# Performance work log

Measured on AMD Instinct MI355X. Metric: run time of the kernel, lower is better.

## Reference

```python
import jax, jax.numpy as jnp
import numpy as np

FEAT_DIM, PART_DIM, N_PARTS, N_EXPERTS, N_ALT = 384, 256, 8, 4, 4
CLUSTER_TEMP = 0.07
EXPERT_WARMUP = 8


def _ln(x, g, b, eps=1e-5):
    mu = x.mean(-1, keepdims=True)
    var = ((x - mu) ** 2).mean(-1, keepdims=True)
    return (x - mu) * jax.lax.rsqrt(var + eps) * g + b


def _l2norm(x, eps=1e-12):
    n = jnp.sqrt((x * x).sum(-1, keepdims=True))
    return x / jnp.maximum(n, eps)


def _gelu(x):
    return jax.nn.gelu(x, approximate=False)


def setup_inputs() -> dict:
    key = jax.random.key(0)
    ks = jax.random.split(key, 32)
    B, N = 256, 576
    s = lambda k, shp, sc=0.02: jax.random.normal(k, shp, jnp.float32) * sc
    inp = {
        'patch_features': jax.random.normal(ks[0], (B, N, FEAT_DIM), jnp.float32),
        'alt_idx': jax.random.randint(ks[1], (B,), 0, N_ALT, jnp.int32),
        'epoch': 0,
        # feat_proj: Linear(384,256) + LayerNorm(256) + GELU
        'w_proj': s(ks[2], (FEAT_DIM, PART_DIM)), 'b_proj': jnp.zeros((PART_DIM,)),
        'ln1_g': jnp.ones((PART_DIM,)), 'ln1_b': jnp.zeros((PART_DIM,)),
        # expert prototypes [E, K, D]
        'protos': s(ks[3], (N_EXPERTS, N_PARTS, PART_DIM)),
        # router
        'r_alt_emb': s(ks[4], (N_ALT, 64), 1.0),
        'r_wf': s(ks[5], (PART_DIM, 64)), 'r_bf': jnp.zeros((64,)),
        'r_w1': s(ks[6], (128, 64)), 'r_b1': jnp.zeros((64,)),
        'r_w2': s(ks[7], (64, N_EXPERTS)), 'r_b2': jnp.zeros((N_EXPERTS,)),
        # refine: LN + Linear(256,512) + GELU + Linear(512,256)
        'ref_ln_g': jnp.ones((PART_DIM,)), 'ref_ln_b': jnp.zeros((PART_DIM,)),
        'ref_w1': s(ks[8], (PART_DIM, 2 * PART_DIM)), 'ref_b1': jnp.zeros((2 * PART_DIM,)),
        'ref_w2': s(ks[9], (2 * PART_DIM, PART_DIM)), 'ref_b2': jnp.zeros((PART_DIM,)),
        # salience head: Linear(256,64)+GELU+Linear(64,1)+Sigmoid
        'sal_w1': s(ks[10], (PART_DIM, 64)), 'sal_b1': jnp.zeros((64,)),
        'sal_w2': s(ks[11], (64, 1)), 'sal_b2': jnp.zeros((1,)),
    }
    return inp


def reference(patch_features, alt_idx, epoch, w_proj, b_proj, ln1_g, ln1_b, protos,
              r_alt_emb, r_wf, r_bf, r_w1, r_b1, r_w2, r_b2,
              ref_ln_g, ref_ln_b, ref_w1, ref_b1, ref_w2, ref_b2,
              sal_w1, sal_b1, sal_w2, sal_b2):
    # --- feat projection ---
    feat = _gelu(_ln(patch_features @ w_proj + b_proj, ln1_g, ln1_b))  # [B,N,D]
    feat_stats = feat.mean(axis=1)  # [B,D]

    # --- router (AltitudeExpertRouter) ---
    warm = min(epoch / max(EXPERT_WARMUP, 1), 1.0)
    router_temp = 2.0 * (1.0 - warm) + 0.5 * warm
    f = jax.nn.relu(feat_stats @ r_wf + r_bf)            # [B,64]
    a = r_alt_emb[alt_idx]                               # [B,64]
    h = jax.nn.relu(jnp.concatenate([f, a], -1) @ r_w1 + r_b1)
    logits = (h @ r_w2 + r_b2) / router_temp             # [B,E]
    gate_weights = jax.nn.softmax(logits, axis=-1)

    # --- blended prototypes + soft assignment ---
    prototypes = jnp.einsum('be,ekd->bkd', gate_weights, protos)  # [B,K,D]
    sim = jnp.einsum('bnd,bkd->bnk', _l2norm(feat), _l2norm(prototypes)) / CLUSTER_TEMP
    assign = jax.nn.softmax(sim, axis=-1)                # [B,N,K]

    assign_t = jnp.swapaxes(assign, 1, 2)                # [B,K,N]
    mass = jnp.maximum(assign_t.sum(-1, keepdims=True), 1e-6)
    part_feat = jnp.einsum('bkn,bnd->bkd', assign_t, feat) / mass

    # --- refine residual ---
    r = _ln(part_feat, ref_ln_g, ref_ln_b)
    r = _gelu(r @ ref_w1 + ref_b1) @ ref_w2 + ref_b2
    part_feat = part_feat + r

    # --- salience ---
    salience = jax.nn.sigmoid(_gelu(part_feat @ sal_w1 + sal_b1) @ sal_w2 + sal_b2)[..., 0]

    return part_feat, assign, salience, feat, gate_weights


if __name__ == '__main__':
    out = reference(**setup_inputs())
    for o in out:
        print(o.shape, o.dtype)
```

## Files before the change

### kernel.cpp

```cpp
#include <hip/hip_runtime.h>
#include <hip/hip_bf16.h>
#include <math.h>

#define B_ 256
#define N_ 576
#define F_ 384
#define D_ 256
#define K_ 8

#define OFF_PART   0
#define OFF_ASSIGN 524288
#define OFF_SAL    1703936
#define OFF_FEAT   1705984
#define OFF_GATE   39454720

#define WS_STATS   0
#define WS_MACC    65536
#define WS_MASS    589824
#define WS_PROTON  591872
#define WS_BTW     1116160

using s16x8 = __attribute__((ext_vector_type(8))) short;
using f32x4 = __attribute__((ext_vector_type(4))) float;

__device__ __forceinline__ float gelu_exact(float x) {
    return 0.5f * x * (1.0f + erff(x * 0.70710678118654752f));
}

__device__ __forceinline__ unsigned short f2b(float f) {
    __hip_bfloat16 h = __float2bfloat16(f);
    unsigned short u;
    __builtin_memcpy(&u, &h, 2);
    return u;
}

__global__ void k0_zero(float* __restrict__ p, int n) {
    int i = blockIdx.x * blockDim.x + threadIdx.x;
    if (i < n) p[i] = 0.f;
}

__global__ void kB_conv(const float* __restrict__ w, unsigned short* __restrict__ bt) {
    int k = threadIdx.x;
    int n = blockIdx.x;
    bt[n * 384 + k] = f2b(w[k * 256 + n]);
}

__global__ __launch_bounds__(256, 3) void k1_pipe(
    const float* __restrict__ patch, const unsigned short* __restrict__ btw,
    const float* __restrict__ bias, const float* __restrict__ g,
    const float* __restrict__ bb, float* __restrict__ feat,
    float* __restrict__ stats)
{
    __shared__ __align__(16) unsigned short As[64 * 72];
    __shared__ __align__(16) unsigned short Bs[256 * 72];
    __shared__ float rsum[4][64];
    __shared__ float rsq[4][64];
    __shared__ float muS[64], rsS[64];

    const int t = threadIdx.x;
    const int w = t >> 6;
    const int lane = t & 63;
    const int l15 = lane & 15;
    const int l4 = lane >> 4;
    const size_t rowbase = (size_t)blockIdx.x * 64;
    const int bidx = blockIdx.x / 9;

    f32x4 acc[4][4];
#pragma unroll
    for (int m = 0; m < 4; ++m)
#pragma unroll
        for (int n = 0; n < 4; ++n)
            acc[m][n] = (f32x4){0.f, 0.f, 0.f, 0.f};

    const int ar = t >> 2;
    const int ak = (t & 3) * 16;
    const int brr = t >> 3;
    const int bk = (t & 7) * 8;

    const float* aptr = patch + (rowbase + ar) * F_ + ak;
    const unsigned short* bptr = btw + (size_t)brr * F_ + bk;

    float4 pa[4];
    s16x8 pb[8];

#pragma unroll
    for (int i = 0; i < 4; ++i) pa[i] = *(const float4*)(aptr + 4 * i);
#pragma unroll
    for (int p = 0; p < 8; ++p) pb[p] = *(const s16x8*)(bptr + (size_t)(32 * p) * F_);

    for (int c = 0; c < 6; ++c) {
        __syncthreads();
        {
            s16x8 c0, c1;
            c0[0] = (short)f2b(pa[0].x); c0[1] = (short)f2b(pa[0].y);
            c0[2] = (short)f2b(pa[0].z); c0[3] = (short)f2b(pa[0].w);
            c0[4] = (short)f2b(pa[1].x); c0[5] = (short)f2b(pa[1].y);
            c0[6] = (short)f2b(pa[1].z); c0[7] = (short)f2b(pa[1].w);
            c1[0] = (short)f2b(pa[2].x); c1[1] = (short)f2b(pa[2].y);
            c1[2] = (short)f2b(pa[2].z); c1[3] = (short)f2b(pa[2].w);
            c1[4] = (short)f2b(pa[3].x); c1[5] = (short)f2b(pa[3].y);
            c1[6] = (short)f2b(pa[3].z); c1[7] = (short)f2b(pa[3].w);
            *(s16x8*)&As[ar * 72 + ak] = c0;
            *(s16x8*)&As[ar * 72 + ak + 8] = c1;
#pragma unroll
            for (int p = 0; p < 8; ++p)
                *(s16x8*)&Bs[(brr + 32 * p) * 72 + bk] = pb[p];
        }
        __syncthreads();
        if (c < 5) {
            const int k1 = (c + 1) * 64;
#pragma unroll
            for (int i = 0; i < 4; ++i) pa[i] = *(const float4*)(aptr + k1 + 4 * i);
#pragma unroll
            for (int p = 0; p < 8; ++p) pb[p] = *(const s16x8*)(bptr + (size_t)(32 * p) * F_ + k1);
        }
#pragma unroll
        for (int kk = 0; kk < 2; ++kk) {
            const int kb = kk * 32 + l4 * 8;
            s16x8 afr[4], bfr[4];
#pragma unroll
            for (int m = 0; m < 4; ++m)
                afr[m] = *(const s16x8*)&As[(m * 16 + l15) * 72 + kb];
#pragma unroll
            for (int n = 0; n < 4; ++n)
                bfr[n] = *(const s16x8*)&Bs[(w * 64 + n * 16 + l15) * 72 + kb];
#pragma unroll
            for (int m = 0; m < 4; ++m)
#pragma unroll
                for (int n = 0; n < 4; ++n)
                    acc[m][n] = __builtin_amdgcn_mfma_f32_16x16x32_bf16(afr[m], bfr[n], acc[m][n], 0, 0, 0);
        }
    }

    float bv[4], gv[4], bbv[4];
#pragma unroll
    for (int n = 0; n < 4; ++n) {
        int col = w * 64 + n * 16 + l15;
        bv[n] = bias[col]; gv[n] = g[col]; bbv[n] = bb[col];
    }
#pragma unroll
    for (int m = 0; m < 4; ++m)
#pragma unroll
        for (int n = 0; n < 4; ++n)
#pragma unroll
            for (int r = 0; r < 4; ++r)
                acc[m][n][r] += bv[n];

    float ps[4][4], p2[4][4];
#pragma unroll
    for (int m = 0; m < 4; ++m)
#pragma unroll
        for (int r = 0; r < 4; ++r) {
            float s = 0.f, s2 = 0.f;
#pragma unroll
            for (int n = 0; n < 4; ++n) {
                float x = acc[m][n][r];
                s += x; s2 += x * x;
            }
            ps[m][r] = s; p2[m][r] = s2;
        }
#pragma unroll
    for (int m = 0; m < 4; ++m)
#pragma unroll
        for (int r = 0; r < 4; ++r) {
#pragma unroll
            for (int msk = 1; msk < 16; msk <<= 1) {
                ps[m][r] += __shfl_xor(ps[m][r], msk);
                p2[m][r] += __shfl_xor(p2[m][r], msk);
            }
        }
    if (l15 == 0) {
#pragma unroll
        for (int m = 0; m < 4; ++m)
#pragma unroll
            for (int r = 0; r < 4; ++r) {
                int row = m * 16 + l4 * 4 + r;
                rsum[w][row] = ps[m][r];
                rsq[w][row] = p2[m][r];
            }
    }
    __syncthreads();
    if (t < 64) {
        float s = rsum[0][t] + rsum[1][t] + rsum[2][t] + rsum[3][t];
        float q = rsq[0][t] + rsq[1][t] + rsq[2][t] + rsq[3][t];
        float mean = s * (1.f / 256.f);
        float var = q * (1.f / 256.f) - mean * mean;
        muS[t] = mean;
        rsS[t] = rsqrtf(var + 1e-5f);
    }
    __syncthreads();

    float cst[4] = {0.f, 0.f, 0.f, 0.f};
#pragma unroll
    for (int m = 0; m < 4; ++m)
#pragma unroll
        for (int r = 0; r < 4; ++r) {
            int row = m * 16 + l4 * 4 + r;
            float mu = muS[row], ri = rsS[row];
            float* fp = feat + (rowbase + row) * 256;
#pragma unroll
            for (int n = 0; n < 4; ++n) {
                int col = w * 64 + n * 16 + l15;
                float x = acc[m][n][r];
                float y = (x - mu) * ri * gv[n] + bbv[n];
                float z = gelu_exact(y);
                fp[col] = z;
                cst[n] += z;
            }
        }
#pragma unroll
    for (int n = 0; n < 4; ++n) {
        cst[n] += __shfl_xor(cst[n], 16);
        cst[n] += __shfl_xor(cst[n], 32);
    }
    if (l4 == 0) {
#pragma unroll
        for (int n = 0; n < 4; ++n)
            atomicAdd(&stats[bidx * 256 + w * 64 + n * 16 + l15], cst[n]);
    }
}

__global__ __launch_bounds__(256) void k3_router(
    const float* __restrict__ stats, const int* __restrict__ alt_idx,
    const int* __restrict__ epoch_p,
    const float* __restrict__ r_alt_emb, const float* __restrict__ r_wf,
    const float* __restrict__ r_bf, const float* __restrict__ r_w1,
    const float* __restrict__ r_b1, const float* __restrict__ r_w2,
    const float* __restrict__ r_b2, const float* __restrict__ protos,
    float* __restrict__ gate_out, float* __restrict__ proto_n)
{
    __shared__ float fs[256];
    __shared__ float cv[128];
    __shared__ float hb[64];
    __shared__ float lg[4];
    __shared__ float gate[4];
    __shared__ float pl[8 * 260];
    __shared__ float nrm[8];
    const int t = threadIdx.x, b = blockIdx.x;
    fs[t] = stats[b * D_ + t] * (1.f / (float)N_);
    __syncthreads();
    if (t < 64) {
        float a = 0.f;
        for (int d = 0; d < 256; ++d) a += fs[d] * r_wf[d * 64 + t];
        cv[t] = fmaxf(a + r_bf[t], 0.f);
    } else if (t < 128) {
        int alt = alt_idx[b];
        cv[t] = r_alt_emb[alt * 64 + (t - 64)];
    }
    __syncthreads();
    if (t < 64) {
        float a = 0.f;
        for (int d = 0; d < 128; ++d) a += cv[d] * r_w1[d * 64 + t];
        hb[t] = fmaxf(a + r_b1[t], 0.f);
    }
    __syncthreads();
    if (t < 4) {
        float a = 0.f;
        for (int d = 0; d < 64; ++d) a += hb[d] * r_w2[d * 4 + t];
        int ep = epoch_p[0];
        float warm = fminf((float)ep * (1.f / 8.f), 1.f);
        float temp = 2.f * (1.f - warm) + 0.5f * warm;
        lg[t] = (a + r_b2[t]) / temp;
    }
    __syncthreads();
    if (t == 0) {
        float m = fmaxf(fmaxf(lg[0], lg[1]), fmaxf(lg[2], lg[3]));
        float e0 = expf(lg[0] - m), e1 = expf(lg[1] - m);
        float e2 = expf(lg[2] - m), e3 = expf(lg[3] - m);
        float s = e0 + e1 + e2 + e3;
        gate[0] = e0 / s; gate[1] = e1 / s; gate[2] = e2 / s; gate[3] = e3 / s;
    }
    __syncthreads();
    if (t < 4) gate_out[b * 4 + t] = gate[t];
    float g0 = gate[0], g1 = gate[1], g2 = gate[2], g3 = gate[3];
#pragma unroll
    for (int k = 0; k < 8; ++k) {
        float p = g0 * protos[(0 * 8 + k) * 256 + t] + g1 * protos[(1 * 8 + k) * 256 + t]
                + g2 * protos[(2 * 8 + k) * 256 + t] + g3 * protos[(3 * 8 + k) * 256 + t];
        pl[k * 260 + t] = p;
    }
    __syncthreads();
    const int wave = t >> 6, lane = t & 63;
#pragma unroll
    for (int kk = 0; kk < 2; ++kk) {
        int k = wave * 2 + kk;
        float4 v = *(const float4*)(&pl[k * 260 + lane * 4]);
        float s2 = v.x * v.x + v.y * v.y + v.z * v.z + v.w * v.w;
#pragma unroll
        for (int m = 1; m < 64; m <<= 1) s2 += __shfl_xor(s2, m);
        if (lane == 0) nrm[k] = 1.f / fmaxf(sqrtf(s2), 1e-12f);
    }
    __syncthreads();
#pragma unroll
    for (int k = 0; k < 8; ++k)
        proto_n[((size_t)(b * 8 + k)) * 256 + t] = pl[k * 260 + t] * nrm[k];
}

__global__ __launch_bounds__(256) void k4_part(
    const float* __restrict__ feat, const float* __restrict__ proto_n,
    float* __restrict__ assign_out, float* __restrict__ macc_ws,
    float* __restrict__ mass_ws)
{
    __shared__ float pp[8 * 260];
    __shared__ float ft[16 * 260];
    __shared__ float asg[16 * 8];
    __shared__ float inrm[16];
    const int t = threadIdx.x, b = blockIdx.y;
    const int wave = t >> 6, lane = t & 63;
#pragma unroll
    for (int k = 0; k < 8; ++k) pp[k * 260 + t] = proto_n[((size_t)(b * 8 + k)) * 256 + t];
    float macc[8], mass[8];
#pragma unroll
    for (int k = 0; k < 8; ++k) { macc[k] = 0.f; mass[k] = 0.f; }
    const int sn = t >> 4;
    const int sk = (t >> 1) & 7;
    const int hf = t & 1;
    const int lc = (t & 15) * 4;
    const int t0 = blockIdx.x * 9;
    for (int tile = t0; tile < t0 + 9; ++tile) {
        int n0 = tile * 16;
        __syncthreads();
        const float* fsrc = feat + ((size_t)(b * N_ + n0 + sn) * D_) + lc;
#pragma unroll
        for (int i = 0; i < 4; ++i) {
            float4 v = *(const float4*)(fsrc + 64 * i);
            *(float4*)(&ft[sn * 260 + lc + 64 * i]) = v;
        }
        __syncthreads();
#pragma unroll
        for (int rr = 0; rr < 4; ++rr) {
            int n = wave * 4 + rr;
            float4 v = *(const float4*)(&ft[n * 260 + lane * 4]);
            float s2 = v.x * v.x + v.y * v.y + v.z * v.z + v.w * v.w;
#pragma unroll
            for (int m = 1; m < 64; m <<= 1) s2 += __shfl_xor(s2, m);
            if (lane == 0) inrm[n] = 1.f / fmaxf(sqrtf(s2), 1e-12f);
        }
        __syncthreads();
        {
            const float4* fp = (const float4*)(&ft[sn * 260 + hf * 128]);
            const float4* qp = (const float4*)(&pp[sk * 260 + hf * 128]);
            float a = 0.f;
#pragma unroll 8
            for (int dd = 0; dd < 32; ++dd) {
                float4 fv = fp[dd], qv = qp[dd];
                a += fv.x * qv.x + fv.y * qv.y + fv.z * qv.z + fv.w * qv.w;
            }
            a += __shfl_xor(a, 1);
            float sim = a * inrm[sn] * (1.f / 0.07f);
            float m = sim;
            m = fmaxf(m, __shfl_xor(m, 2));
            m = fmaxf(m, __shfl_xor(m, 4));
            m = fmaxf(m, __shfl_xor(m, 8));
            float p = expf(sim - m);
            float s = p;
            s += __shfl_xor(s, 2);
            s += __shfl_xor(s, 4);
            s += __shfl_xor(s, 8);
            float av = p / s;
            if (hf == 0) assign_out[((size_t)(b * N_ + n0 + sn)) * 8 + sk] = av;
            asg[sn * 8 + sk] = av;
        }
        __syncthreads();
#pragma unroll 4
        for (int nn = 0; nn < 16; ++nn) {
            float4 a03 = *(const float4*)(&asg[nn * 8]);
            float4 a47 = *(const float4*)(&asg[nn * 8 + 4]);
            float fv = ft[nn * 260 + t];
            macc[0] += a03.x * fv; macc[1] += a03.y * fv;
            macc[2] += a03.z * fv; macc[3] += a03.w * fv;
            macc[4] += a47.x * fv; macc[5] += a47.y * fv;
            macc[6] += a47.z * fv; macc[7] += a47.w * fv;
            mass[0] += a03.x; mass[1] += a03.y; mass[2] += a03.z; mass[3] += a03.w;
            mass[4] += a47.x; mass[5] += a47.y; mass[6] += a47.z; mass[7] += a47.w;
        }
    }
#pragma unroll
    for (int k = 0; k < 8; ++k)
        atomicAdd(&macc_ws[((size_t)(b * 8 + k)) * 256 + t], macc[k]);
    if (t == 0) {
        atomicAdd(&mass_ws[b * 8 + 0], mass[0]);
        atomicAdd(&mass_ws[b * 8 + 1], mass[1]);
        atomicAdd(&mass_ws[b * 8 + 2], mass[2]);
        atomicAdd(&mass_ws[b * 8 + 3], mass[3]);
        atomicAdd(&mass_ws[b * 8 + 4], mass[4]);
        atomicAdd(&mass_ws[b * 8 + 5], mass[5]);
        atomicAdd(&mass_ws[b * 8 + 6], mass[6]);
        atomicAdd(&mass_ws[b * 8 + 7], mass[7]);
    }
}

__global__ __launch_bounds__(256) void k5_refine(
    const float* __restrict__ macc_ws, const float* __restrict__ mass_ws,
    const float* __restrict__ ref_ln_g, const float* __restrict__ ref_ln_b,
    const float* __restrict__ ref_w1, const float* __restrict__ ref_b1,
    const float* __restrict__ ref_w2, const float* __restrict__ ref_b2,
    const float* __restrict__ sal_w1, const float* __restrict__ sal_b1,
    const float* __restrict__ sal_w2, const float* __restrict__ sal_b2,
    float* __restrict__ part_out, float* __restrict__ sal_out)
{
    __shared__ float raw[8 * 256];
    __shared__ float rn[8 * 256];
    __shared__ float h1[8 * 512];
    __shared__ float pf[8 * 256];
    __shared__ float s1[8 * 64];
    __shared__ float mu[8], rs[8];
    const int t = threadIdx.x, b = blockIdx.x;
    const int wave = t >> 6, lane = t & 63;
#pragma unroll
    for (int r = 0; r < 8; ++r) {
        float mm = fmaxf(mass_ws[b * 8 + r], 1e-6f);
        raw[r * 256 + t] = macc_ws[((size_t)(b * 8 + r)) * 256 + t] / mm;
    }
    __syncthreads();
#pragma unroll
    for (int rr = 0; rr < 2; ++rr) {
        int r = wave + rr * 4;
        float4 v = *(const float4*)(&raw[r * 256 + lane * 4]);
        float s = v.x + v.y + v.z + v.w;
        float s2 = v.x * v.x + v.y * v.y + v.z * v.z + v.w * v.w;
#pragma unroll
        for (int m = 1; m < 64; m <<= 1) { s += __shfl_xor(s, m); s2 += __shfl_xor(s2, m); }
        if (lane == 0) {
            float mean = s * (1.f / 256.f);
            float var = s2 * (1.f / 256.f) - mean * mean;
            mu[r] = mean;
            rs[r] = rsqrtf(var + 1e-5f);
        }
    }
    __syncthreads();
    {
        float gg = ref_ln_g[t], bbv = ref_ln_b[t];
#pragma unroll
        for (int r = 0; r < 8; ++r) {
            float x = raw[r * 256 + t];
            rn[r * 256 + t] = (x - mu[r]) * rs[r] * gg + bbv;
        }
    }
    __syncthreads();
    {
        float acca[8], accb[8];
#pragma unroll
        for (int r = 0; r < 8; ++r) { acca[r] = 0.f; accb[r] = 0.f; }
        for (int d = 0; d < 256; d += 4) {
            float4 rv[8];
#pragma unroll
            for (int r = 0; r < 8; ++r) rv[r] = *(const float4*)(&rn[r * 256 + d]);
            float wa0 = ref_w1[(size_t)(d + 0) * 512 + t], wb0 = ref_w1[(size_t)(d + 0) * 512 + t + 256];
            float wa1 = ref_w1[(size_t)(d + 1) * 512 + t], wb1 = ref_w1[(size_t)(d + 1) * 512 + t + 256];
            float wa2 = ref_w1[(size_t)(d + 2) * 512 + t], wb2 = ref_w1[(size_t)(d + 2) * 512 + t + 256];
            float wa3 = ref_w1[(size_t)(d + 3) * 512 + t], wb3 = ref_w1[(size_t)(d + 3) * 512 + t + 256];
#pragma unroll
            for (int r = 0; r < 8; ++r) {
                acca[r] += rv[r].x * wa0 + rv[r].y * wa1 + rv[r].z * wa2 + rv[r].w * wa3;
                accb[r] += rv[r].x * wb0 + rv[r].y * wb1 + rv[r].z * wb2 + rv[r].w * wb3;
            }
        }
        float b1a = ref_b1[t], b1b = ref_b1[t + 256];
#pragma unroll
        for (int r = 0; r < 8; ++r) {
            h1[r * 512 + t] = gelu_exact(acca[r] + b1a);
            h1[r * 512 + t + 256] = gelu_exact(accb[r] + b1b);
        }
    }
    __syncthreads();
    {
        float acc2[8];
#pragma unroll
        for (int r = 0; r < 8; ++r) acc2[r] = 0.f;
        for (int d = 0; d < 512; d += 4) {
            float4 hv[8];
#pragma unroll
            for (int r = 0; r < 8; ++r) hv[r] = *(const float4*)(&h1[r * 512 + d]);
            float w0 = ref_w2[(size_t)(d + 0) * 256 + t];
            float w1v = ref_w2[(size_t)(d + 1) * 256 + t];
            float w2v = ref_w2[(size_t)(d + 2) * 256 + t];
            float w3v = ref_w2[(size_t)(d + 3) * 256 + t];
#pragma unroll
            for (int r = 0; r < 8; ++r)
                acc2[r] += hv[r].x * w0 + hv[r].y * w1v + hv[r].z * w2v + hv[r].w * w3v;
        }
        float b2v = ref_b2[t];
#pragma unroll
        for (int r = 0; r < 8; ++r) {
            float v = raw[r * 256 + t] + acc2[r] + b2v;
            part_out[((size_t)(b * 8 + r)) * 256 + t] = v;
            pf[r * 256 + t] = v;
        }
    }
    __syncthreads();
    for (int o = t; o < 512; o += 256) {
        int r = o >> 6, j = o & 63;
        float a = 0.f;
        for (int d = 0; d < 256; d += 4) {
            float4 v = *(const float4*)(&pf[r * 256 + d]);
            a += v.x * sal_w1[(d + 0) * 64 + j] + v.y * sal_w1[(d + 1) * 64 + j]
               + v.z * sal_w1[(d + 2) * 64 + j] + v.w * sal_w1[(d + 3) * 64 + j];
        }
        s1[o] = gelu_exact(a + sal_b1[j]);
    }
    __syncthreads();
    if (t < 8) {
        float a = 0.f;
#pragma unroll 8
        for (int d = 0; d < 64; ++d) a += s1[t * 64 + d] * sal_w2[d];
        float x = a + sal_b2[0];
        sal_out[b * 8 + t] = 1.f / (1.f + expf(-x));
    }
}

extern "C" void kernel_launch(void* const* d_in, const int* in_sizes, int n_in,
                              void* d_out, int out_size, void* d_ws, size_t ws_size,
                              hipStream_t stream) {
    const float* patch    = (const float*)d_in[0];
    const int*   alt_idx  = (const int*)d_in[1];
    const int*   epoch    = (const int*)d_in[2];
    const float* w_proj   = (const float*)d_in[3];
    const float* b_proj   = (const float*)d_in[4];
    const float* ln1_g    = (const float*)d_in[5];
    const float* ln1_b    = (const float*)d_in[6];
    const float* protos   = (const float*)d_in[7];
    const float* r_alt    = (const float*)d_in[8];
    const float* r_wf     = (const float*)d_in[9];
    const float* r_bf     = (const float*)d_in[10];
    const float* r_w1     = (const float*)d_in[11];
    const float* r_b1     = (const float*)d_in[12];
    const float* r_w2     = (const float*)d_in[13];
    const float* r_b2     = (const float*)d_in[14];
    const float* ref_ln_g = (const float*)d_in[15];
    const float* ref_ln_b = (const float*)d_in[16];
    const float* ref_w1   = (const float*)d_in[17];
    const float* ref_b1   = (const float*)d_in[18];
    const float* ref_w2   = (const float*)d_in[19];
    const float* ref_b2   = (const float*)d_in[20];
    const float* sal_w1   = (const float*)d_in[21];
    const float* sal_b1   = (const float*)d_in[22];
    const float* sal_w2   = (const float*)d_in[23];
    const float* sal_b2   = (const float*)d_in[24];

    float* out = (float*)d_out;
    float* wsf = (float*)d_ws;
    float* stats   = wsf + WS_STATS;
    float* macc    = wsf + WS_MACC;
    float* mass    = wsf + WS_MASS;
    float* proto_n = wsf + WS_PROTON;
    unsigned short* btw = (unsigned short*)(wsf + WS_BTW);

    k0_zero<<<dim3((65536 + 524288 + 2048 + 255) / 256), dim3(256), 0, stream>>>(stats, 65536 + 524288 + 2048);
    kB_conv<<<dim3(256), dim3(384), 0, stream>>>(w_proj, btw);
    k1_pipe<<<dim3(2304), dim3(256), 0, stream>>>(patch, btw, b_proj, ln1_g, ln1_b,
                                                  out + OFF_FEAT, stats);
    k3_router<<<dim3(256), dim3(256), 0, stream>>>(stats, alt_idx, epoch, r_alt, r_wf, r_bf,
                                                   r_w1, r_b1, r_w2, r_b2, protos,
                                                   out + OFF_GATE, proto_n);
    k4_part<<<dim3(4, 256), dim3(256), 0, stream>>>(out + OFF_FEAT, proto_n,
                                                    out + OFF_ASSIGN, macc, mass);
    k5_refine<<<dim3(256), dim3(256), 0, stream>>>(macc, mass,
                                                   ref_ln_g, ref_ln_b, ref_w1, ref_b1,
                                                   ref_w2, ref_b2, sal_w1, sal_b1, sal_w2, sal_b2,
                                                   out + OFF_PART, out + OFF_SAL);
}
```

Before: 306.5 us.

## Stage full A tile in swizzled LDS and stream B fragments from global

The projection GEMM kernel now converts the whole 64x384 A tile to bf16 once into XOR-swizzled shared memory. B fragments are read straight from global/L2 into registers with double buffering, which removes the per-K-chunk LDS staging of B and the two barriers per chunk. Separately, the part kernel computes per-prototype mass with 8 threads per tile instead of every thread, which cuts redundant adds. The trade-off is a larger LDS footprint (48KB for A) that may limit occupancy, plus more global traffic for B that relies on cache hits.

```diff
diff --git a/kernel.cpp b/kernel.cpp
--- a/kernel.cpp
+++ b/kernel.cpp
@@ -45,14 +45,13 @@
     bt[n * 384 + k] = f2b(w[k * 256 + n]);
 }
 
-__global__ __launch_bounds__(256, 3) void k1_pipe(
+__global__ __launch_bounds__(256, 3) void k1_rs(
     const float* __restrict__ patch, const unsigned short* __restrict__ btw,
     const float* __restrict__ bias, const float* __restrict__ g,
     const float* __restrict__ bb, float* __restrict__ feat,
     float* __restrict__ stats)
 {
-    __shared__ __align__(16) unsigned short As[64 * 72];
-    __shared__ __align__(16) unsigned short Bs[256 * 72];
+    __shared__ __align__(16) unsigned short As[64 * 384];
     __shared__ float rsum[4][64];
     __shared__ float rsq[4][64];
     __shared__ float muS[64], rsS[64];
@@ -65,6 +64,26 @@
     const size_t rowbase = (size_t)blockIdx.x * 64;
     const int bidx = blockIdx.x / 9;
 
+    {
+        const int row = t >> 2, seg = t & 3;
+        const float* src = patch + (rowbase + row) * F_ + seg * 96;
+        char* As_c = (char*)As;
+        const int rbase = row * 768;
+        const int rs7 = (row & 7) << 4;
+#pragma unroll
+        for (int jj = 0; jj < 12; ++jj) {
+            float4 v0 = *(const float4*)(src + jj * 8);
+            float4 v1 = *(const float4*)(src + jj * 8 + 4);
+            s16x8 pk;
+            pk[0] = (short)f2b(v0.x); pk[1] = (short)f2b(v0.y);
+            pk[2] = (short)f2b(v0.z); pk[3] = (short)f2b(v0.w);
+            pk[4] = (short)f2b(v1.x); pk[5] = (short)f2b(v1.y);
+            pk[6] = (short)f2b(v1.z); pk[7] = (short)f2b(v1.w);
+            *(s16x8*)(As_c + rbase + ((seg * 192 + jj * 16) ^ rs7)) = pk;
+        }
+    }
+    __syncthreads();
+
     f32x4 acc[4][4];
 #pragma unroll
     for (int m = 0; m < 4; ++m)
@@ -72,63 +91,46 @@
         for (int n = 0; n < 4; ++n)
             acc[m][n] = (f32x4){0.f, 0.f, 0.f, 0.f};
 
-    const int ar = t >> 2;
-    const int ak = (t & 3) * 16;
-    const int brr = t >> 3;
-    const int bk = (t & 7) * 8;
-
-    const float* aptr = patch + (rowbase + ar) * F_ + ak;
-    const unsigned short* bptr = btw + (size_t)brr * F_ + bk;
-
-    float4 pa[4];
-    s16x8 pb[8];
-
-#pragma unroll
-    for (int i = 0; i < 4; ++i) pa[i] = *(const float4*)(aptr + 4 * i);
-#pragma unroll
-    for (int p = 0; p < 8; ++p) pb[p] = *(const s16x8*)(bptr + (size_t)(32 * p) * F_);
-
-    for (int c = 0; c < 6; ++c) {
-        __syncthreads();
+    const char* As_r = (const char*)As;
+    const int rs7v = (l15 & 7) << 4;
+    const unsigned short* bcol = btw + (size_t)(w * 64 + l15) * F_ + l4 * 8;
+
+    s16x8 pbA[4], pbB[4];
+#pragma unroll
+    for (int n = 0; n < 4; ++n) pbA[n] = *(const s16x8*)(bcol + n * 6144);
+
+#pragma unroll
+    for (int kk = 0; kk < 6; ++kk) {
+        const int ks0 = 2 * kk, ks1 = ks0 + 1;
+#pragma unroll
+        for (int n = 0; n < 4; ++n)
+            pbB[n] = *(const s16x8*)(bcol + n * 6144 + ks1 * 32);
         {
-            s16x8 c0, c1;
-            c0[0] = (short)f2b(pa[0].x); c0[1] = (short)f2b(pa[0].y);
-            c0[2] = (short)f2b(pa[0].z); c0[3] = (short)f2b(pa[0].w);
-            c0[4] = (short)f2b(pa[1].x); c0[5] = (short)f2b(pa[1].y);
-            c0[6] = (short)f2b(pa[1].z); c0[7] = (short)f2b(pa[1].w);
-            c1[0] = (short)f2b(pa[2].x); c1[1] = (short)f2b(pa[2].y);
-            c1[2] = (short)f2b(pa[2].z); c1[3] = (short)f2b(pa[2].w);
-            c1[4] = (short)f2b(pa[3].x); c1[5] = (short)f2b(pa[3].y);
-            c1[6] = (short)f2b(pa[3].z); c1[7] = (short)f2b(pa[3].w);
-            *(s16x8*)&As[ar * 72 + ak] = c0;
-            *(s16x8*)&As[ar * 72 + ak + 8] = c1;
-#pragma unroll
-            for (int p = 0; p < 8; ++p)
-                *(s16x8*)&Bs[(brr + 32 * p) * 72 + bk] = pb[p];
-        }
-        __syncthreads();
-        if (c < 5) {
-            const int k1 = (c + 1) * 64;
-#pragma unroll
-            for (int i = 0; i < 4; ++i) pa[i] = *(const float4*)(aptr + k1 + 4 * i);
-#pragma unroll
-            for (int p = 0; p < 8; ++p) pb[p] = *(const s16x8*)(bptr + (size_t)(32 * p) * F_ + k1);
-        }
-#pragma unroll
-        for (int kk = 0; kk < 2; ++kk) {
-            const int kb = kk * 32 + l4 * 8;
-            s16x8 afr[4], bfr[4];
+            s16x8 afr[4];
 #pragma unroll
             for (int m = 0; m < 4; ++m)
-                afr[m] = *(const s16x8*)&As[(m * 16 + l15) * 72 + kb];
+                afr[m] = *(const s16x8*)(As_r + (m * 16 + l15) * 768 + ((ks0 * 64 + l4 * 16) ^ rs7v));
+#pragma unroll
+            for (int m = 0; m < 4; ++m)
+#pragma unroll
+                for (int n = 0; n < 4; ++n)
+                    acc[m][n] = __builtin_amdgcn_mfma_f32_16x16x32_bf16(afr[m], pbA[n], acc[m][n], 0, 0, 0);
+        }
+        if (kk < 5) {
 #pragma unroll
             for (int n = 0; n < 4; ++n)
-                bfr[n] = *(const s16x8*)&Bs[(w * 64 + n * 16 + l15) * 72 + kb];
+                pbA[n] = *(const s16x8*)(bcol + n * 6144 + (ks0 + 2) * 32);
+        }
+        {
+            s16x8 afr[4];
 #pragma unroll
             for (int m = 0; m < 4; ++m)
+                afr[m] = *(const s16x8*)(As_r + (m * 16 + l15) * 768 + ((ks1 * 64 + l4 * 16) ^ rs7v));
+#pragma unroll
+            for (int m = 0; m < 4; ++m)
 #pragma unroll
                 for (int n = 0; n < 4; ++n)
-                    acc[m][n] = __builtin_amdgcn_mfma_f32_16x16x32_bf16(afr[m], bfr[n], acc[m][n], 0, 0, 0);
+                    acc[m][n] = __builtin_amdgcn_mfma_f32_16x16x32_bf16(afr[m], pbB[n], acc[m][n], 0, 0, 0);
         }
     }
 
@@ -309,9 +311,10 @@
     const int wave = t >> 6, lane = t & 63;
 #pragma unroll
     for (int k = 0; k < 8; ++k) pp[k * 260 + t] = proto_n[((size_t)(b * 8 + k)) * 256 + t];
-    float macc[8], mass[8];
-#pragma unroll
-    for (int k = 0; k < 8; ++k) { macc[k] = 0.f; mass[k] = 0.f; }
+    float macc[8];
+#pragma unroll
+    for (int k = 0; k < 8; ++k) macc[k] = 0.f;
+    float massr = 0.f;
     const int sn = t >> 4;
     const int sk = (t >> 1) & 7;
     const int hf = t & 1;
@@ -362,6 +365,10 @@
             asg[sn * 8 + sk] = av;
         }
         __syncthreads();
+        if (t < 8) {
+#pragma unroll
+            for (int nn = 0; nn < 16; ++nn) massr += asg[nn * 8 + t];
+        }
 #pragma unroll 4
         for (int nn = 0; nn < 16; ++nn) {
             float4 a03 = *(const float4*)(&asg[nn * 8]);
@@ -371,23 +378,12 @@
             macc[2] += a03.z * fv; macc[3] += a03.w * fv;
             macc[4] += a47.x * fv; macc[5] += a47.y * fv;
             macc[6] += a47.z * fv; macc[7] += a47.w * fv;
-            mass[0] += a03.x; mass[1] += a03.y; mass[2] += a03.z; mass[3] += a03.w;
-            mass[4] += a47.x; mass[5] += a47.y; mass[6] += a47.z; mass[7] += a47.w;
         }
     }
 #pragma unroll
     for (int k = 0; k < 8; ++k)
         atomicAdd(&macc_ws[((size_t)(b * 8 + k)) * 256 + t], macc[k]);
-    if (t == 0) {
-        atomicAdd(&mass_ws[b * 8 + 0], mass[0]);
-        atomicAdd(&mass_ws[b * 8 + 1], mass[1]);
-        atomicAdd(&mass_ws[b * 8 + 2], mass[2]);
-        atomicAdd(&mass_ws[b * 8 + 3], mass[3]);
-        atomicAdd(&mass_ws[b * 8 + 4], mass[4]);
-        atomicAdd(&mass_ws[b * 8 + 5], mass[5]);
-        atomicAdd(&mass_ws[b * 8 + 6], mass[6]);
-        atomicAdd(&mass_ws[b * 8 + 7], mass[7]);
-    }
+    if (t < 8) atomicAdd(&mass_ws[b * 8 + t], massr);
 }
 
 __global__ __launch_bounds__(256) void k5_refine(
@@ -548,8 +544,8 @@
 
     k0_zero<<<dim3((65536 + 524288 + 2048 + 255) / 256), dim3(256), 0, stream>>>(stats, 65536 + 524288 + 2048);
     kB_conv<<<dim3(256), dim3(384), 0, stream>>>(w_proj, btw);
-    k1_pipe<<<dim3(2304), dim3(256), 0, stream>>>(patch, btw, b_proj, ln1_g, ln1_b,
-                                                  out + OFF_FEAT, stats);
+    k1_rs<<<dim3(2304), dim3(256), 0, stream>>>(patch, btw, b_proj, ln1_g, ln1_b,
+                                                out + OFF_FEAT, stats);
     k3_router<<<dim3(256), dim3(256), 0, stream>>>(stats, alt_idx, epoch, r_alt, r_wf, r_bf,
                                                    r_w1, r_b1, r_w2, r_b2, protos,
                                                    out + OFF_GATE, proto_n);
```

After: 322.1 us. +5.1%, slower.

## Split projection GEMM from LayerNorm/GELU pass and precompute feature inverse norms

Applied to the files above, without the earlier changes.

The fused GEMM+LN+GELU kernel is split in two. The GEMM now stages its bias-added output through shared memory and writes it with coalesced float4 stores. A separate row-wise kernel then applies LayerNorm and GELU in place, accumulates the per-batch column sums, and also stores each row's inverse L2 norm. The partition kernel reads those precomputed norms instead of recomputing them, and the mass reduction is moved from per-thread register accumulation to a few threads reading the shared assignment tile. In exchange the feature tensor (about 150 MB) makes an extra round trip through global memory, plus one more kernel launch.

```diff
diff --git a/kernel.cpp b/kernel.cpp
--- a/kernel.cpp
+++ b/kernel.cpp
@@ -18,7 +18,8 @@
 #define WS_MACC    65536
 #define WS_MASS    589824
 #define WS_PROTON  591872
-#define WS_BTW     1116160
+#define WS_INVN    1116160
+#define WS_BTW     1263616
 
 using s16x8 = __attribute__((ext_vector_type(8))) short;
 using f32x4 = __attribute__((ext_vector_type(4))) float;
@@ -45,17 +46,12 @@
     bt[n * 384 + k] = f2b(w[k * 256 + n]);
 }
 
-__global__ __launch_bounds__(256, 3) void k1_pipe(
+__global__ __launch_bounds__(256, 3) void k1g_gemm(
     const float* __restrict__ patch, const unsigned short* __restrict__ btw,
-    const float* __restrict__ bias, const float* __restrict__ g,
-    const float* __restrict__ bb, float* __restrict__ feat,
-    float* __restrict__ stats)
+    const float* __restrict__ bias, float* __restrict__ feat_raw)
 {
     __shared__ __align__(16) unsigned short As[64 * 72];
     __shared__ __align__(16) unsigned short Bs[256 * 72];
-    __shared__ float rsum[4][64];
-    __shared__ float rsq[4][64];
-    __shared__ float muS[64], rsS[64];
 
     const int t = threadIdx.x;
     const int w = t >> 6;
@@ -63,7 +59,6 @@
     const int l15 = lane & 15;
     const int l4 = lane >> 4;
     const size_t rowbase = (size_t)blockIdx.x * 64;
-    const int bidx = blockIdx.x / 9;
 
     f32x4 acc[4][4];
 #pragma unroll
@@ -132,92 +127,83 @@
         }
     }
 
-    float bv[4], gv[4], bbv[4];
-#pragma unroll
-    for (int n = 0; n < 4; ++n) {
-        int col = w * 64 + n * 16 + l15;
-        bv[n] = bias[col]; gv[n] = g[col]; bbv[n] = bb[col];
-    }
-#pragma unroll
-    for (int m = 0; m < 4; ++m)
-#pragma unroll
-        for (int n = 0; n < 4; ++n)
-#pragma unroll
-            for (int r = 0; r < 4; ++r)
-                acc[m][n][r] += bv[n];
-
-    float ps[4][4], p2[4][4];
-#pragma unroll
-    for (int m = 0; m < 4; ++m)
-#pragma unroll
-        for (int r = 0; r < 4; ++r) {
-            float s = 0.f, s2 = 0.f;
-#pragma unroll
-            for (int n = 0; n < 4; ++n) {
-                float x = acc[m][n][r];
-                s += x; s2 += x * x;
-            }
-            ps[m][r] = s; p2[m][r] = s2;
-        }
-#pragma unroll
-    for (int m = 0; m < 4; ++m)
-#pragma unroll
-        for (int r = 0; r < 4; ++r) {
-#pragma unroll
-            for (int msk = 1; msk < 16; msk <<= 1) {
-                ps[m][r] += __shfl_xor(ps[m][r], msk);
-                p2[m][r] += __shfl_xor(p2[m][r], msk);
-            }
-        }
-    if (l15 == 0) {
-#pragma unroll
-        for (int m = 0; m < 4; ++m)
-#pragma unroll
-            for (int r = 0; r < 4; ++r) {
-                int row = m * 16 + l4 * 4 + r;
-                rsum[w][row] = ps[m][r];
-                rsq[w][row] = p2[m][r];
-            }
-    }
-    __syncthreads();
-    if (t < 64) {
-        float s = rsum[0][t] + rsum[1][t] + rsum[2][t] + rsum[3][t];
-        float q = rsq[0][t] + rsq[1][t] + rsq[2][t] + rsq[3][t];
-        float mean = s * (1.f / 256.f);
-        float var = q * (1.f / 256.f) - mean * mean;
-        muS[t] = mean;
-        rsS[t] = rsqrtf(var + 1e-5f);
-    }
-    __syncthreads();
-
-    float cst[4] = {0.f, 0.f, 0.f, 0.f};
-#pragma unroll
-    for (int m = 0; m < 4; ++m)
-#pragma unroll
-        for (int r = 0; r < 4; ++r) {
-            int row = m * 16 + l4 * 4 + r;
-            float mu = muS[row], ri = rsS[row];
-            float* fp = feat + (rowbase + row) * 256;
-#pragma unroll
-            for (int n = 0; n < 4; ++n) {
-                int col = w * 64 + n * 16 + l15;
-                float x = acc[m][n][r];
-                float y = (x - mu) * ri * gv[n] + bbv[n];
-                float z = gelu_exact(y);
-                fp[col] = z;
-                cst[n] += z;
-            }
-        }
-#pragma unroll
-    for (int n = 0; n < 4; ++n) {
-        cst[n] += __shfl_xor(cst[n], 16);
-        cst[n] += __shfl_xor(cst[n], 32);
-    }
-    if (l4 == 0) {
-#pragma unroll
-        for (int n = 0; n < 4; ++n)
-            atomicAdd(&stats[bidx * 256 + w * 64 + n * 16 + l15], cst[n]);
-    }
+    float bv[4];
+#pragma unroll
+    for (int n = 0; n < 4; ++n) bv[n] = bias[w * 64 + n * 16 + l15];
+    float* T = (float*)Bs;
+#pragma unroll
+    for (int h = 0; h < 2; ++h) {
+        __syncthreads();
+#pragma unroll
+        for (int m2 = 0; m2 < 2; ++m2) {
+            const int m = h * 2 + m2;
+#pragma unroll
+            for (int n = 0; n < 4; ++n)
+#pragma unroll
+                for (int r = 0; r < 4; ++r)
+                    T[(m2 * 16 + l4 * 4 + r) * 260 + w * 64 + n * 16 + l15] = acc[m][n][r] + bv[n];
+        }
+        __syncthreads();
+#pragma unroll
+        for (int p = 0; p < 8; ++p) {
+            const int R = p * 4 + w;
+            float4 v = *(const float4*)&T[R * 260 + lane * 4];
+            *(float4*)&feat_raw[(rowbase + h * 32 + R) * 256 + lane * 4] = v;
+        }
+    }
+}
+
+__global__ __launch_bounds__(256) void k1c_ln(
+    float* __restrict__ feat, const float* __restrict__ g,
+    const float* __restrict__ bb, float* __restrict__ stats,
+    float* __restrict__ invn)
+{
+    const int t = threadIdx.x;
+    const int w = t >> 6;
+    const int lane = t & 63;
+    const size_t rowbase = (size_t)blockIdx.x * 64;
+    const int bidx = blockIdx.x / 9;
+
+    float4 gq = *(const float4*)&g[lane * 4];
+    float4 bq = *(const float4*)&bb[lane * 4];
+    float cst0 = 0.f, cst1 = 0.f, cst2 = 0.f, cst3 = 0.f;
+
+    size_t row = rowbase + w;
+    float4 v = *(const float4*)&feat[row * 256 + lane * 4];
+#pragma unroll 4
+    for (int pass = 0; pass < 16; ++pass) {
+        float4 cur = v;
+        size_t crow = row;
+        if (pass < 15) {
+            row += 4;
+            v = *(const float4*)&feat[row * 256 + lane * 4];
+        }
+        float s = cur.x + cur.y + cur.z + cur.w;
+        float s2 = cur.x * cur.x + cur.y * cur.y + cur.z * cur.z + cur.w * cur.w;
+#pragma unroll
+        for (int msk = 1; msk < 64; msk <<= 1) {
+            s += __shfl_xor(s, msk);
+            s2 += __shfl_xor(s2, msk);
+        }
+        float mu = s * (1.f / 256.f);
+        float var = s2 * (1.f / 256.f) - mu * mu;
+        float ri = rsqrtf(var + 1e-5f);
+        float z0 = gelu_exact((cur.x - mu) * ri * gq.x + bq.x);
+        float z1 = gelu_exact((cur.y - mu) * ri * gq.y + bq.y);
+        float z2 = gelu_exact((cur.z - mu) * ri * gq.z + bq.z);
+        float z3 = gelu_exact((cur.w - mu) * ri * gq.w + bq.w);
+        float4 zv = {z0, z1, z2, z3};
+        *(float4*)&feat[crow * 256 + lane * 4] = zv;
+        cst0 += z0; cst1 += z1; cst2 += z2; cst3 += z3;
+        float q2 = z0 * z0 + z1 * z1 + z2 * z2 + z3 * z3;
+#pragma unroll
+        for (int msk = 1; msk < 64; msk <<= 1) q2 += __shfl_xor(q2, msk);
+        if (lane == 0) invn[crow] = 1.f / fmaxf(sqrtf(q2), 1e-12f);
+    }
+    atomicAdd(&stats[bidx * 256 + lane * 4 + 0], cst0);
+    atomicAdd(&stats[bidx * 256 + lane * 4 + 1], cst1);
+    atomicAdd(&stats[bidx * 256 + lane * 4 + 2], cst2);
+    atomicAdd(&stats[bidx * 256 + lane * 4 + 3], cst3);
 }
 
 __global__ __launch_bounds__(256) void k3_router(
@@ -298,6 +284,7 @@
 
 __global__ __launch_bounds__(256) void k4_part(
     const float* __restrict__ feat, const float* __restrict__ proto_n,
+    const float* __restrict__ invn,
     float* __restrict__ assign_out, float* __restrict__ macc_ws,
     float* __restrict__ mass_ws)
 {
@@ -306,12 +293,12 @@
     __shared__ float asg[16 * 8];
     __shared__ float inrm[16];
     const int t = threadIdx.x, b = blockIdx.y;
-    const int wave = t >> 6, lane = t & 63;
 #pragma unroll
     for (int k = 0; k < 8; ++k) pp[k * 260 + t] = proto_n[((size_t)(b * 8 + k)) * 256 + t];
-    float macc[8], mass[8];
-#pragma unroll
-    for (int k = 0; k < 8; ++k) { macc[k] = 0.f; mass[k] = 0.f; }
+    float macc[8];
+#pragma unroll
+    for (int k = 0; k < 8; ++k) macc[k] = 0.f;
+    float massr = 0.f;
     const int sn = t >> 4;
     const int sk = (t >> 1) & 7;
     const int hf = t & 1;
@@ -326,16 +313,7 @@
             float4 v = *(const float4*)(fsrc + 64 * i);
             *(float4*)(&ft[sn * 260 + lc + 64 * i]) = v;
         }
-        __syncthreads();
-#pragma unroll
-        for (int rr = 0; rr < 4; ++rr) {
-            int n = wave * 4 + rr;
-            float4 v = *(const float4*)(&ft[n * 260 + lane * 4]);
-            float s2 = v.x * v.x + v.y * v.y + v.z * v.z + v.w * v.w;
-#pragma unroll
-            for (int m = 1; m < 64; m <<= 1) s2 += __shfl_xor(s2, m);
-            if (lane == 0) inrm[n] = 1.f / fmaxf(sqrtf(s2), 1e-12f);
-        }
+        if (t < 16) inrm[t] = invn[(size_t)b * N_ + n0 + t];
         __syncthreads();
         {
             const float4* fp = (const float4*)(&ft[sn * 260 + hf * 128]);
@@ -362,6 +340,10 @@
             asg[sn * 8 + sk] = av;
         }
         __syncthreads();
+        if (t < 8) {
+#pragma unroll
+            for (int nn = 0; nn < 16; ++nn) massr += asg[nn * 8 + t];
+        }
 #pragma unroll 4
         for (int nn = 0; nn < 16; ++nn) {
             float4 a03 = *(const float4*)(&asg[nn * 8]);
@@ -371,23 +353,12 @@
             macc[2] += a03.z * fv; macc[3] += a03.w * fv;
             macc[4] += a47.x * fv; macc[5] += a47.y * fv;
             macc[6] += a47.z * fv; macc[7] += a47.w * fv;
-            mass[0] += a03.x; mass[1] += a03.y; mass[2] += a03.z; mass[3] += a03.w;
-            mass[4] += a47.x; mass[5] += a47.y; mass[6] += a47.z; mass[7] += a47.w;
         }
     }
 #pragma unroll
     for (int k = 0; k < 8; ++k)
         atomicAdd(&macc_ws[((size_t)(b * 8 + k)) * 256 + t], macc[k]);
-    if (t == 0) {
-        atomicAdd(&mass_ws[b * 8 + 0], mass[0]);
-        atomicAdd(&mass_ws[b * 8 + 1], mass[1]);
-        atomicAdd(&mass_ws[b * 8 + 2], mass[2]);
-        atomicAdd(&mass_ws[b * 8 + 3], mass[3]);
-        atomicAdd(&mass_ws[b * 8 + 4], mass[4]);
-        atomicAdd(&mass_ws[b * 8 + 5], mass[5]);
-        atomicAdd(&mass_ws[b * 8 + 6], mass[6]);
-        atomicAdd(&mass_ws[b * 8 + 7], mass[7]);
-    }
+    if (t < 8) atomicAdd(&mass_ws[b * 8 + t], massr);
 }
 
 __global__ __launch_bounds__(256) void k5_refine(
@@ -544,16 +515,17 @@
     float* macc    = wsf + WS_MACC;
     float* mass    = wsf + WS_MASS;
     float* proto_n = wsf + WS_PROTON;
+    float* invn    = wsf + WS_INVN;
     unsigned short* btw = (unsigned short*)(wsf + WS_BTW);
 
     k0_zero<<<dim3((65536 + 524288 + 2048 + 255) / 256), dim3(256), 0, stream>>>(stats, 65536 + 524288 + 2048);
     kB_conv<<<dim3(256), dim3(384), 0, stream>>>(w_proj, btw);
-    k1_pipe<<<dim3(2304), dim3(256), 0, stream>>>(patch, btw, b_proj, ln1_g, ln1_b,
-                                                  out + OFF_FEAT, stats);
+    k1g_gemm<<<dim3(2304), dim3(256), 0, stream>>>(patch, btw, b_proj, out + OFF_FEAT);
+    k1c_ln<<<dim3(2304), dim3(256), 0, stream>>>(out + OFF_FEAT, ln1_g, ln1_b, stats, invn);
     k3_router<<<dim3(256), dim3(256), 0, stream>>>(stats, alt_idx, epoch, r_alt, r_wf, r_bf,
                                                    r_w1, r_b1, r_w2, r_b2, protos,
                                                    out + OFF_GATE, proto_n);
-    k4_part<<<dim3(4, 256), dim3(256), 0, stream>>>(out + OFF_FEAT, proto_n,
+    k4_part<<<dim3(4, 256), dim3(256), 0, stream>>>(out + OFF_FEAT, proto_n, invn,
                                                     out + OFF_ASSIGN, macc, mass);
     k5_refine<<<dim3(256), dim3(256), 0, stream>>>(macc, mass,
                                                    ref_ln_g, ref_ln_b, ref_w1, ref_b1,
```

Result: slower. 346.2 us (+13.0%).

## Fuse row L2-norm into projection kernel and coalesce feat stores via LDS

Applied to the files above, without the earlier changes.

The projection kernel now computes each feature row's inverse L2 norm while the values are still in registers and writes it to a workspace buffer. It also stages the output tile through shared memory so feat is written with full-row float4 stores instead of strided scalar stores. The assignment kernel reads the precomputed norms instead of recomputing them with a barrier and shuffle reductions, and its mass accumulation moves to eight threads reading the shared assign tile. This adds extra barriers and shared-memory traffic to the projection kernel and costs a small extra workspace write and read.

```diff
diff --git a/kernel.cpp b/kernel.cpp
--- a/kernel.cpp
+++ b/kernel.cpp
@@ -18,7 +18,8 @@
 #define WS_MACC    65536
 #define WS_MASS    589824
 #define WS_PROTON  591872
-#define WS_BTW     1116160
+#define WS_INVN    1116160
+#define WS_BTW     1263616
 
 using s16x8 = __attribute__((ext_vector_type(8))) short;
 using f32x4 = __attribute__((ext_vector_type(4))) float;
@@ -45,11 +46,11 @@
     bt[n * 384 + k] = f2b(w[k * 256 + n]);
 }
 
-__global__ __launch_bounds__(256, 3) void k1_pipe(
+__global__ __launch_bounds__(256, 3) void k1_zt(
     const float* __restrict__ patch, const unsigned short* __restrict__ btw,
     const float* __restrict__ bias, const float* __restrict__ g,
     const float* __restrict__ bb, float* __restrict__ feat,
-    float* __restrict__ stats)
+    float* __restrict__ stats, float* __restrict__ invn)
 {
     __shared__ __align__(16) unsigned short As[64 * 72];
     __shared__ __align__(16) unsigned short Bs[256 * 72];
@@ -191,21 +192,25 @@
     __syncthreads();
 
     float cst[4] = {0.f, 0.f, 0.f, 0.f};
+    float q2[4][4];
+#pragma unroll
+    for (int m = 0; m < 4; ++m)
+#pragma unroll
+        for (int r = 0; r < 4; ++r) q2[m][r] = 0.f;
 #pragma unroll
     for (int m = 0; m < 4; ++m)
 #pragma unroll
         for (int r = 0; r < 4; ++r) {
             int row = m * 16 + l4 * 4 + r;
             float mu = muS[row], ri = rsS[row];
-            float* fp = feat + (rowbase + row) * 256;
 #pragma unroll
             for (int n = 0; n < 4; ++n) {
-                int col = w * 64 + n * 16 + l15;
                 float x = acc[m][n][r];
                 float y = (x - mu) * ri * gv[n] + bbv[n];
                 float z = gelu_exact(y);
-                fp[col] = z;
+                acc[m][n][r] = z;
                 cst[n] += z;
+                q2[m][r] += z * z;
             }
         }
 #pragma unroll
@@ -217,6 +222,42 @@
 #pragma unroll
         for (int n = 0; n < 4; ++n)
             atomicAdd(&stats[bidx * 256 + w * 64 + n * 16 + l15], cst[n]);
+    }
+#pragma unroll
+    for (int m = 0; m < 4; ++m)
+#pragma unroll
+        for (int r = 0; r < 4; ++r) {
+            float q = q2[m][r];
+            q += __shfl_xor(q, 1); q += __shfl_xor(q, 2);
+            q += __shfl_xor(q, 4); q += __shfl_xor(q, 8);
+            if (l15 == 0) rsum[w][m * 16 + l4 * 4 + r] = q;
+        }
+    __syncthreads();
+    if (t < 64) {
+        float tot = rsum[0][t] + rsum[1][t] + rsum[2][t] + rsum[3][t];
+        invn[rowbase + t] = 1.f / fmaxf(sqrtf(tot), 1e-12f);
+    }
+
+    float* T = (float*)Bs;
+#pragma unroll
+    for (int h = 0; h < 2; ++h) {
+        __syncthreads();
+#pragma unroll
+        for (int m2 = 0; m2 < 2; ++m2) {
+            const int m = h * 2 + m2;
+#pragma unroll
+            for (int n = 0; n < 4; ++n)
+#pragma unroll
+                for (int r = 0; r < 4; ++r)
+                    T[(m2 * 16 + l4 * 4 + r) * 260 + w * 64 + n * 16 + l15] = acc[m][n][r];
+        }
+        __syncthreads();
+#pragma unroll
+        for (int p = 0; p < 8; ++p) {
+            const int R = p * 4 + w;
+            float4 v = *(const float4*)&T[R * 260 + lane * 4];
+            *(float4*)&feat[(rowbase + h * 32 + R) * 256 + lane * 4] = v;
+        }
     }
 }
 
@@ -298,6 +339,7 @@
 
 __global__ __launch_bounds__(256) void k4_part(
     const float* __restrict__ feat, const float* __restrict__ proto_n,
+    const float* __restrict__ invn,
     float* __restrict__ assign_out, float* __restrict__ macc_ws,
     float* __restrict__ mass_ws)
 {
@@ -306,12 +348,12 @@
     __shared__ float asg[16 * 8];
     __shared__ float inrm[16];
     const int t = threadIdx.x, b = blockIdx.y;
-    const int wave = t >> 6, lane = t & 63;
 #pragma unroll
     for (int k = 0; k < 8; ++k) pp[k * 260 + t] = proto_n[((size_t)(b * 8 + k)) * 256 + t];
-    float macc[8], mass[8];
-#pragma unroll
-    for (int k = 0; k < 8; ++k) { macc[k] = 0.f; mass[k] = 0.f; }
+    float macc[8];
+#pragma unroll
+    for (int k = 0; k < 8; ++k) macc[k] = 0.f;
+    float massr = 0.f;
     const int sn = t >> 4;
     const int sk = (t >> 1) & 7;
     const int hf = t & 1;
@@ -326,16 +368,7 @@
             float4 v = *(const float4*)(fsrc + 64 * i);
             *(float4*)(&ft[sn * 260 + lc + 64 * i]) = v;
         }
-        __syncthreads();
-#pragma unroll
-        for (int rr = 0; rr < 4; ++rr) {
-            int n = wave * 4 + rr;
-            float4 v = *(const float4*)(&ft[n * 260 + lane * 4]);
-            float s2 = v.x * v.x + v.y * v.y + v.z * v.z + v.w * v.w;
-#pragma unroll
-            for (int m = 1; m < 64; m <<= 1) s2 += __shfl_xor(s2, m);
-            if (lane == 0) inrm[n] = 1.f / fmaxf(sqrtf(s2), 1e-12f);
-        }
+        if (t < 16) inrm[t] = invn[(size_t)b * N_ + n0 + t];
         __syncthreads();
         {
             const float4* fp = (const float4*)(&ft[sn * 260 + hf * 128]);
@@ -362,6 +395,10 @@
             asg[sn * 8 + sk] = av;
         }
         __syncthreads();
+        if (t < 8) {
+#pragma unroll
+            for (int nn = 0; nn < 16; ++nn) massr += asg[nn * 8 + t];
+        }
 #pragma unroll 4
         for (int nn = 0; nn < 16; ++nn) {
             float4 a03 = *(const float4*)(&asg[nn * 8]);
@@ -371,23 +408,12 @@
             macc[2] += a03.z * fv; macc[3] += a03.w * fv;
             macc[4] += a47.x * fv; macc[5] += a47.y * fv;
             macc[6] += a47.z * fv; macc[7] += a47.w * fv;
-            mass[0] += a03.x; mass[1] += a03.y; mass[2] += a03.z; mass[3] += a03.w;
-            mass[4] += a47.x; mass[5] += a47.y; mass[6] += a47.z; mass[7] += a47.w;
         }
     }
 #pragma unroll
     for (int k = 0; k < 8; ++k)
         atomicAdd(&macc_ws[((size_t)(b * 8 + k)) * 256 + t], macc[k]);
-    if (t == 0) {
-        atomicAdd(&mass_ws[b * 8 + 0], mass[0]);
-        atomicAdd(&mass_ws[b * 8 + 1], mass[1]);
-        atomicAdd(&mass_ws[b * 8 + 2], mass[2]);
-        atomicAdd(&mass_ws[b * 8 + 3], mass[3]);
-        atomicAdd(&mass_ws[b * 8 + 4], mass[4]);
-        atomicAdd(&mass_ws[b * 8 + 5], mass[5]);
-        atomicAdd(&mass_ws[b * 8 + 6], mass[6]);
-        atomicAdd(&mass_ws[b * 8 + 7], mass[7]);
-    }
+    if (t < 8) atomicAdd(&mass_ws[b * 8 + t], massr);
 }
 
 __global__ __launch_bounds__(256) void k5_refine(
@@ -544,16 +570,17 @@
     float* macc    = wsf + WS_MACC;
     float* mass    = wsf + WS_MASS;
     float* proto_n = wsf + WS_PROTON;
+    float* invn    = wsf + WS_INVN;
     unsigned short* btw = (unsigned short*)(wsf + WS_BTW);
 
     k0_zero<<<dim3((65536 + 524288 + 2048 + 255) / 256), dim3(256), 0, stream>>>(stats, 65536 + 524288 + 2048);
     kB_conv<<<dim3(256), dim3(384), 0, stream>>>(w_proj, btw);
-    k1_pipe<<<dim3(2304), dim3(256), 0, stream>>>(patch, btw, b_proj, ln1_g, ln1_b,
-                                                  out + OFF_FEAT, stats);
+    k1_zt<<<dim3(2304), dim3(256), 0, stream>>>(patch, btw, b_proj, ln1_g, ln1_b,
+                                                out + OFF_FEAT, stats, invn);
     k3_router<<<dim3(256), dim3(256), 0, stream>>>(stats, alt_idx, epoch, r_alt, r_wf, r_bf,
                                                    r_w1, r_b1, r_w2, r_b2, protos,
                                                    out + OFF_GATE, proto_n);
-    k4_part<<<dim3(4, 256), dim3(256), 0, stream>>>(out + OFF_FEAT, proto_n,
+    k4_part<<<dim3(4, 256), dim3(256), 0, stream>>>(out + OFF_FEAT, proto_n, invn,
                                                     out + OFF_ASSIGN, macc, mass);
     k5_refine<<<dim3(256), dim3(256), 0, stream>>>(macc, mass,
                                                    ref_ln_g, ref_ln_b, ref_w1, ref_b1,
```

After: 328.6 us. 1.07x slower.
